# Kernel optimization log

Hardware: AMD Instinct MI355X
Metric: run time of the kernel (lower is better)

The kernel has to match this reference:

```python
import jax, jax.numpy as jnp
import numpy as np

B, S, H = 32, 512, 768          # batch, encoder seq len, hidden size
W, G = 128, 4                   # max words per example, max tokens per word group
NH, HD, FF, NL, NLAB = 4, 192, 2048, 2, 6  # heads, head dim, ffn dim, layers, labels
EPS = 1e-5


def setup_inputs() -> dict:
    key = jax.random.key(0)
    ks = jax.random.split(key, 16)
    s = 0.02
    hidden = jax.random.normal(ks[0], (B, S, H), jnp.float32)
    word_token_idx = jax.random.randint(ks[1], (B, W, G), 0, S).astype(jnp.int32)
    glen = jax.random.randint(ks[2], (B, W), 1, G + 1)
    group_token_mask = jnp.arange(G)[None, None, :] < glen[:, :, None]  # [B,W,G] bool
    nwords = jax.random.randint(ks[3], (B,), W // 2, W + 1)
    word_valid = jnp.arange(W)[None, :] < nwords[:, None]               # [B,W] bool
    return {
        'hidden': hidden,
        'word_token_idx': word_token_idx,
        'group_token_mask': group_token_mask,
        'word_valid': word_valid,
        'qkv_w': jax.random.normal(ks[4], (NL, 3 * H, H), jnp.float32) * s,
        'qkv_b': jnp.zeros((NL, 3 * H), jnp.float32),
        'out_w': jax.random.normal(ks[5], (NL, H, H), jnp.float32) * s,
        'out_b': jnp.zeros((NL, H), jnp.float32),
        'ff1_w': jax.random.normal(ks[6], (NL, FF, H), jnp.float32) * s,
        'ff1_b': jnp.zeros((NL, FF), jnp.float32),
        'ff2_w': jax.random.normal(ks[7], (NL, H, FF), jnp.float32) * s,
        'ff2_b': jnp.zeros((NL, H), jnp.float32),
        'ln1_s': jnp.ones((NL, H), jnp.float32),
        'ln1_b': jnp.zeros((NL, H), jnp.float32),
        'ln2_s': jnp.ones((NL, H), jnp.float32),
        'ln2_b': jnp.zeros((NL, H), jnp.float32),
        'cls_w': jax.random.normal(ks[8], (NLAB, H), jnp.float32) * s,
        'cls_b': jnp.zeros((NLAB,), jnp.float32),
    }


def _ln(x, s, b):
    m = x.mean(-1, keepdims=True)
    v = ((x - m) ** 2).mean(-1, keepdims=True)
    return (x - m) * jax.lax.rsqrt(v + EPS) * s + b


def reference(hidden, word_token_idx, group_token_mask, word_valid,
              qkv_w, qkv_b, out_w, out_b, ff1_w, ff1_b, ff2_w, ff2_b,
              ln1_s, ln1_b, ln2_s, ln2_b, cls_w, cls_b):
    dt = hidden.dtype
    # ragged per-word gather + masked mean over each subword group: [B,W,G,H]
    gathered = jax.vmap(lambda h, i: h[i])(hidden, word_token_idx)
    gm = group_token_mask[..., None].astype(dt)
    wemb = (gathered * gm).sum(2) / jnp.maximum(gm.sum(2), 1.0)   # [B,W,H]
    # invalid (padded) words are zero, matching torch pad_sequence zero-padding
    wemb = wemb * word_valid[..., None].astype(dt)
    cls = hidden[:, 0, :]
    x = jnp.concatenate([cls[:, None, :], wemb], axis=1)          # [B, W+1, H]
    # key padding mask: True = padded position; CLS slot always valid
    pad = jnp.concatenate([jnp.zeros((B, 1), bool), ~word_valid], axis=1)
    neg = jnp.finfo(dt).min
    Lw = W + 1
    scale = 1.0 / np.sqrt(HD)
    for l in range(NL):  # 2 post-norm TransformerEncoder layers
        qkv = x @ qkv_w[l].T + qkv_b[l]
        q, k, v = jnp.split(qkv, 3, axis=-1)
        q = q.reshape(B, Lw, NH, HD).transpose(0, 2, 1, 3)
        k = k.reshape(B, Lw, NH, HD).transpose(0, 2, 1, 3)
        v = v.reshape(B, Lw, NH, HD).transpose(0, 2, 1, 3)
        scores = jnp.einsum('bhqd,bhkd->bhqk', q, k) * scale
        scores = jnp.where(pad[:, None, None, :], neg, scores)
        a = jax.nn.softmax(scores, axis=-1)
        ctx = jnp.einsum('bhqk,bhkd->bhqd', a, v).transpose(0, 2, 1, 3).reshape(B, Lw, H)
        attn = ctx @ out_w[l].T + out_b[l]
        x = _ln(x + attn, ln1_s[l], ln1_b[l])
        h1 = jax.nn.relu(x @ ff1_w[l].T + ff1_b[l])
        x = _ln(x + h1 @ ff2_w[l].T + ff2_b[l], ln2_s[l], ln2_b[l])
    pooled = x[:, 0, :]
    logits = pooled @ cls_w.T + cls_b
    return (logits, pooled)
```

## Files before the change

### kernel.cpp

```cpp
#include <hip/hip_runtime.h>
#include <hip/hip_bf16.h>
#include <math.h>

#define B_  32
#define S_  512
#define H_  768
#define W_  128
#define G_  4
#define LW  129
#define NH_ 4
#define HD_ 192
#define FF_ 2048
#define NL_ 2
#define NLAB_ 6
#define M_   (B_ * LW)
#define MPAD 4224
#define EPS_ 1e-5f
#define SCALE_ 0.07216878364870323f

#define TP 192
#define KP 160
#define KR 144
#define KLD 200
#define PLD 168

#define QW_SZ (3 * H_ * H_)
#define OW_SZ (H_ * H_)
#define F1_SZ (FF_ * H_)
#define F2_SZ (H_ * FF_)
#define WL_SZ (QW_SZ + OW_SZ + F1_SZ + F2_SZ)

typedef __bf16 bf16_8 __attribute__((ext_vector_type(8)));
typedef float  f32x4  __attribute__((ext_vector_type(4)));
typedef unsigned short ushort8_t __attribute__((ext_vector_type(8)));

__device__ __forceinline__ float b2f(unsigned short u) {
    union { unsigned int i; float f; } c; c.i = ((unsigned int)u) << 16; return c.f;
}
__device__ __forceinline__ unsigned short f2b(float f) {
    union { float f; unsigned int u; } c; c.f = f;
    unsigned int u = c.u;
    return (unsigned short)((u + 0x7FFFu + ((u >> 16) & 1u)) >> 16);
}

__device__ __forceinline__ float wave_sum(float v) {
#pragma unroll
    for (int off = 1; off < 64; off <<= 1) v += __shfl_xor(v, off, 64);
    return v;
}
__device__ __forceinline__ float block_sum(float v, float* red) {
    v = wave_sum(v);
    int wid = threadIdx.x >> 6, lane = threadIdx.x & 63;
    if (lane == 0) red[wid] = v;
    __syncthreads();
    float r = (red[0] + red[1]) + (red[2] + red[3]);
    __syncthreads();
    return r;
}

__global__ __launch_bounds__(256) void build_x_kernel(
    const float* __restrict__ hidden,
    const int*   __restrict__ wti,
    const int*   __restrict__ gmask,
    const int*   __restrict__ wvalid,
    unsigned short* __restrict__ xb)
{
    int t = blockIdx.x;
    int b = blockIdx.y;
    int tid = threadIdx.x;
    if (t >= LW) {
        int pr = M_ + b * 3 + (t - LW);
        size_t xo = (size_t)pr * H_;
#pragma unroll
        for (int i = 0; i < 3; i++) xb[xo + tid + i * 256] = 0;
        return;
    }
    size_t xo = ((size_t)b * LW + t) * H_;
    if (t == 0) {
        const float* src = hidden + (size_t)b * S_ * H_;
#pragma unroll
        for (int i = 0; i < 3; i++) xb[xo + tid + i * 256] = f2b(src[tid + i * 256]);
    } else {
        int w = t - 1;
        int valid = wvalid[b * W_ + w];
        int ids[G_]; float msk[G_]; float cnt = 0.f;
#pragma unroll
        for (int g = 0; g < G_; g++) {
            ids[g] = wti[(b * W_ + w) * G_ + g];
            msk[g] = (gmask[(b * W_ + w) * G_ + g] != 0) ? 1.f : 0.f;
            cnt += msk[g];
        }
        float inv = valid ? (1.f / fmaxf(cnt, 1.f)) : 0.f;
#pragma unroll
        for (int i = 0; i < 3; i++) {
            int c = tid + i * 256;
            float a = 0.f;
#pragma unroll
            for (int g = 0; g < G_; g++)
                a += msk[g] * hidden[((size_t)b * S_ + ids[g]) * H_ + c];
            xb[xo + c] = f2b(a * inv);
        }
    }
}

__global__ __launch_bounds__(256) void cvt_all_kernel(
    const float4* __restrict__ qw, const float4* __restrict__ ow,
    const float4* __restrict__ f1, const float4* __restrict__ f2,
    ushort4* __restrict__ dst)
{
    constexpr int WL4 = WL_SZ / 4;
    int i = blockIdx.x * 256 + threadIdx.x;
    int l = (i < WL4) ? 0 : 1;
    int j = i - l * WL4;
    float4 v;
    if (j < QW_SZ / 4)                          v = qw[l * (QW_SZ / 4) + j];
    else if (j < (QW_SZ + OW_SZ) / 4)           v = ow[l * (OW_SZ / 4) + j - QW_SZ / 4];
    else if (j < (QW_SZ + OW_SZ + F1_SZ) / 4)   v = f1[l * (F1_SZ / 4) + j - (QW_SZ + OW_SZ) / 4];
    else                                        v = f2[l * (F2_SZ / 4) + j - (QW_SZ + OW_SZ + F1_SZ) / 4];
    ushort4 o; o.x = f2b(v.x); o.y = f2b(v.y); o.z = f2b(v.z); o.w = f2b(v.w);
    dst[i] = o;
}

template <int BM, int BN, int BK, int RELU, int OUTBF, int SWZ>
__global__ __launch_bounds__(256) void gemm_mfma(
    const unsigned short* __restrict__ A,
    const unsigned short* __restrict__ Bw,
    const float* __restrict__ bias,
    void* __restrict__ Cout,
    int N, int K)
{
    constexpr int MI  = BM / 32;
    constexpr int NJ  = BN / 32;
    constexpr int CPR = BK / 8;
    constexpr int RPL = 2048 / BK;
    constexpr int SA  = BM * BK / 2048;
    constexpr int SB  = BN * BK / 2048;

    __shared__ __align__(16) unsigned short As[BM * BK];
    __shared__ __align__(16) unsigned short Bs[BN * BK];

    const int tid  = threadIdx.x;
    const int lane = tid & 63;
    const int wid  = tid >> 6;

    int bx = blockIdx.x, by = blockIdx.y;
    if (SWZ) {
        int nx = gridDim.x;
        int total = nx * gridDim.y;
        int id = by * nx + bx;
        int id2 = (id & 7) * (total >> 3) + (id >> 3);
        by = id2 / nx; bx = id2 - by * nx;
    }
    const int bm = by * BM;
    const int bn = bx * BN;

    const int wm = (wid & 1) * (BM / 2);
    const int wn = (wid >> 1) * (BN / 2);
    const int r  = lane & 15;
    const int q8 = lane >> 4;
    const int m8 = r & (CPR - 1);

    const int srow = tid / CPR;
    const int scol = (tid % CPR) ^ (srow & (CPR - 1));
    const unsigned short* Ag = A  + (size_t)(bm + srow) * K + scol * 8;
    const unsigned short* Bg = Bw + (size_t)(bn + srow) * K + scol * 8;

    const bf16_8* Af = (const bf16_8*)As;
    const bf16_8* Bf = (const bf16_8*)Bs;
    int arow[MI], brow[NJ];
#pragma unroll
    for (int i = 0; i < MI; i++) arow[i] = (wm + i * 16 + r) * CPR;
#pragma unroll
    for (int j = 0; j < NJ; j++) brow[j] = (wn + j * 16 + r) * CPR;

    f32x4 acc[MI][NJ];
#pragma unroll
    for (int i = 0; i < MI; i++)
#pragma unroll
        for (int j = 0; j < NJ; j++) acc[i][j] = (f32x4){0.f, 0.f, 0.f, 0.f};

    for (int k0 = 0; k0 < K; k0 += BK) {
#pragma unroll
        for (int s = 0; s < SA; s++)
            __builtin_amdgcn_global_load_lds(
                (const __attribute__((address_space(1))) void*)(Ag + (size_t)(s * RPL) * K + k0),
                (__attribute__((address_space(3))) void*)(As + s * 2048 + tid * 8), 16, 0, 0);
#pragma unroll
        for (int s = 0; s < SB; s++)
            __builtin_amdgcn_global_load_lds(
                (const __attribute__((address_space(1))) void*)(Bg + (size_t)(s * RPL) * K + k0),
                (__attribute__((address_space(3))) void*)(Bs + s * 2048 + tid * 8), 16, 0, 0);
        __syncthreads();
#pragma unroll
        for (int ks = 0; ks < BK / 32; ks++) {
            const int cc = (ks * 4 + q8) ^ m8;
            bf16_8 a[MI], b[NJ];
#pragma unroll
            for (int i = 0; i < MI; i++) a[i] = Af[arow[i] + cc];
#pragma unroll
            for (int j = 0; j < NJ; j++) b[j] = Bf[brow[j] + cc];
#pragma unroll
            for (int i = 0; i < MI; i++)
#pragma unroll
                for (int j = 0; j < NJ; j++)
                    acc[i][j] = __builtin_amdgcn_mfma_f32_16x16x32_bf16(a[i], b[j], acc[i][j], 0, 0, 0);
        }
        __syncthreads();
    }

    int col[NJ]; float bv[NJ];
#pragma unroll
    for (int j = 0; j < NJ; j++) { col[j] = bn + wn + j * 16 + r; bv[j] = bias[col[j]]; }
    const int row0 = bm + wm + ((lane >> 4) << 2);
#pragma unroll
    for (int i = 0; i < MI; i++) {
#pragma unroll
        for (int rg = 0; rg < 4; rg++) {
            size_t rowoff = (size_t)(row0 + i * 16 + rg) * N;
#pragma unroll
            for (int j = 0; j < NJ; j++) {
                float v = acc[i][j][rg] + bv[j];
                if (RELU) v = fmaxf(v, 0.f);
                if (OUTBF) ((unsigned short*)Cout)[rowoff + col[j]] = f2b(v);
                else       ((float*)Cout)[rowoff + col[j]] = v;
            }
        }
    }
}

__global__ __launch_bounds__(256) void vt_kernel(
    const unsigned short* __restrict__ qkv,
    unsigned short* __restrict__ vtb)
{
    __shared__ __align__(16) unsigned short Vs[KR * KLD];
    int bh = blockIdx.x;
    int b = bh >> 2, h = bh & 3;
    int tid = threadIdx.x;
    for (int c = tid; c < KR * 24; c += 256) {
        int t = c / 24, j = c - t * 24;
        ushort8_t v = (ushort8_t){0,0,0,0,0,0,0,0};
        if (t < LW)
            v = *(const ushort8_t*)(qkv + (size_t)(b * LW + t) * (3 * H_) + 2 * H_ + h * HD_ + j * 8);
        *(ushort8_t*)(&Vs[t * KLD + j * 8]) = v;
    }
    __syncthreads();
    size_t obase = (size_t)bh * (HD_ * KP);
    for (int c = tid; c < HD_ * (KP / 4); c += 256) {
        int d = c / (KP / 4), t0 = (c - d * (KP / 4)) * 4;
        ushort4 o;
        o.x = (t0 + 0 < KR) ? Vs[(t0 + 0) * KLD + d] : 0;
        o.y = (t0 + 1 < KR) ? Vs[(t0 + 1) * KLD + d] : 0;
        o.z = (t0 + 2 < KR) ? Vs[(t0 + 2) * KLD + d] : 0;
        o.w = (t0 + 3 < KR) ? Vs[(t0 + 3) * KLD + d] : 0;
        *(ushort4*)(&vtb[obase + (size_t)d * KP + t0]) = o;
    }
}

__global__ __launch_bounds__(256) void attn_fused_kernel(
    const unsigned short* __restrict__ qkv,
    const int*            __restrict__ wvalid,
    const unsigned short* __restrict__ vtb,
    unsigned short*       __restrict__ ctx)
{
    __shared__ __align__(16) unsigned short Ks[KR * KLD];
    __shared__ __align__(16) unsigned short Ps[64 * PLD];
    __shared__ float msk[KR];
    int mb = blockIdx.x;
    int bh = blockIdx.y;
    int b = bh >> 2, h = bh & 3;
    int tid = threadIdx.x, lane = tid & 63, wid = tid >> 6;
    int q = lane >> 4, r = lane & 15;

    for (int c = tid; c < KR * 24; c += 256) {
        int t = c / 24, j = c - t * 24;
        ushort8_t v = (ushort8_t){0,0,0,0,0,0,0,0};
        if (t < LW)
            v = *(const ushort8_t*)(qkv + (size_t)(b * LW + t) * (3 * H_) + H_ + h * HD_ + j * 8);
        *(ushort8_t*)(&Ks[t * KLD + j * 8]) = v;
    }
    if (tid < KR) {
        bool valid = (tid == 0) || (tid <= W_ && wvalid[b * W_ + tid - 1] != 0);
        msk[tid] = valid ? 0.f : -1e30f;
    }
    __syncthreads();

    const int lrow0 = wid * 16;
    const unsigned short* Qp = qkv + ((size_t)(b * LW) + mb * 64 + lrow0 + r) * (3 * H_) + h * HD_;

    f32x4 acc[9];
#pragma unroll
    for (int nt = 0; nt < 9; nt++) acc[nt] = (f32x4){0.f, 0.f, 0.f, 0.f};
    for (int ks = 0; ks < HD_ / 32; ks++) {
        bf16_8 a = *(const bf16_8*)(Qp + ks * 32 + q * 8);
#pragma unroll
        for (int nt = 0; nt < 9; nt++) {
            bf16_8 bfrag = *(const bf16_8*)(&Ks[(nt * 16 + r) * KLD + ks * 32 + q * 8]);
            acc[nt] = __builtin_amdgcn_mfma_f32_16x16x32_bf16(a, bfrag, acc[nt], 0, 0, 0);
        }
    }
    float mk[9];
#pragma unroll
    for (int nt = 0; nt < 9; nt++) mk[nt] = msk[nt * 16 + r];
#pragma unroll
    for (int rg = 0; rg < 4; rg++) {
        float v[9]; float mx = -1e30f;
#pragma unroll
        for (int nt = 0; nt < 9; nt++) { v[nt] = acc[nt][rg] * SCALE_ + mk[nt]; mx = fmaxf(mx, v[nt]); }
#pragma unroll
        for (int off = 1; off < 16; off <<= 1) mx = fmaxf(mx, __shfl_xor(mx, off, 64));
        float s = 0.f;
#pragma unroll
        for (int nt = 0; nt < 9; nt++) { v[nt] = __expf(v[nt] - mx); s += v[nt]; }
#pragma unroll
        for (int off = 1; off < 16; off <<= 1) s += __shfl_xor(s, off, 64);
        float inv = 1.f / s;
        int lr = lrow0 + q * 4 + rg;
#pragma unroll
        for (int nt = 0; nt < 9; nt++)
            Ps[lr * PLD + nt * 16 + r] = f2b(v[nt] * inv);
        Ps[lr * PLD + KR + r] = 0;
    }
    __syncthreads();

    const int wm = (wid & 1) * 32, wn = (wid >> 1) * 96;
    size_t vbase = (size_t)bh * (HD_ * KP);

    f32x4 pacc[2][6];
#pragma unroll
    for (int i = 0; i < 2; i++)
#pragma unroll
        for (int j = 0; j < 6; j++) pacc[i][j] = (f32x4){0.f, 0.f, 0.f, 0.f};

    for (int ks = 0; ks < KP / 32; ks++) {
        bf16_8 a[2], bb[6];
#pragma unroll
        for (int i = 0; i < 2; i++)
            a[i] = *(const bf16_8*)(&Ps[(wm + i * 16 + r) * PLD + ks * 32 + q * 8]);
#pragma unroll
        for (int j = 0; j < 6; j++)
            bb[j] = *(const bf16_8*)(vtb + vbase + (size_t)(wn + j * 16 + r) * KP + ks * 32 + q * 8);
#pragma unroll
        for (int i = 0; i < 2; i++)
#pragma unroll
            for (int j = 0; j < 6; j++)
                pacc[i][j] = __builtin_amdgcn_mfma_f32_16x16x32_bf16(a[i], bb[j], pacc[i][j], 0, 0, 0);
    }

#pragma unroll
    for (int i = 0; i < 2; i++) {
#pragma unroll
        for (int rg = 0; rg < 4; rg++) {
            int tl = mb * 64 + wm + i * 16 + q * 4 + rg;
            if (tl < LW) {
                size_t rowoff = (size_t)(b * LW + tl) * H_ + h * HD_;
#pragma unroll
                for (int j = 0; j < 6; j++)
                    ctx[rowoff + wn + j * 16 + r] = f2b(pacc[i][j][rg]);
            }
        }
    }
}

__global__ __launch_bounds__(256) void add_ln_kernel(
    unsigned short* __restrict__ xb, const unsigned short* __restrict__ res,
    const float* __restrict__ sc, const float* __restrict__ bi)
{
    __shared__ float red[4];
    int row = blockIdx.x;
    int tid = threadIdx.x;
    size_t base = (size_t)row * H_;
    float v[3];
    float sum = 0.f;
#pragma unroll
    for (int i = 0; i < 3; i++) {
        int c = tid + i * 256;
        float t = b2f(xb[base + c]) + b2f(res[base + c]);
        v[i] = t; sum += t;
    }
    sum = block_sum(sum, red);
    float mean = sum * (1.f / H_);
    float var = 0.f;
#pragma unroll
    for (int i = 0; i < 3; i++) { float d = v[i] - mean; var += d * d; }
    var = block_sum(var, red);
    float inv = rsqrtf(var * (1.f / H_) + EPS_);
#pragma unroll
    for (int i = 0; i < 3; i++) {
        int c = tid + i * 256;
        xb[base + c] = f2b((v[i] - mean) * inv * sc[c] + bi[c]);
    }
}

__global__ __launch_bounds__(384) void cls_kernel(
    const unsigned short* __restrict__ xb,
    const float* __restrict__ cls_w, const float* __restrict__ cls_b,
    float* __restrict__ out)
{
    int b = blockIdx.x;
    int tid = threadIdx.x;
    const unsigned short* p = &xb[((size_t)b * LW) * H_];
    for (int c = tid; c < H_; c += 384) out[B_ * NLAB_ + b * H_ + c] = b2f(p[c]);
    int w = tid >> 6, lane = tid & 63;
    if (w < NLAB_) {
        const float* wv = &cls_w[w * H_];
        float acc = 0.f;
#pragma unroll
        for (int i = 0; i < H_ / 64; i++) {
            int c = lane + i * 64;
            acc += b2f(p[c]) * wv[c];
        }
        acc = wave_sum(acc);
        if (lane == 0) out[b * NLAB_ + w] = acc + cls_b[w];
    }
}

extern "C" void kernel_launch(void* const* d_in, const int* in_sizes, int n_in,
                              void* d_out, int out_size, void* d_ws, size_t ws_size,
                              hipStream_t stream) {
    const float* hidden = (const float*)d_in[0];
    const int*   wti    = (const int*)d_in[1];
    const int*   gmask  = (const int*)d_in[2];
    const int*   wvalid = (const int*)d_in[3];
    const float* qkv_w  = (const float*)d_in[4];
    const float* qkv_b  = (const float*)d_in[5];
    const float* out_w  = (const float*)d_in[6];
    const float* out_b  = (const float*)d_in[7];
    const float* ff1_w  = (const float*)d_in[8];
    const float* ff1_b  = (const float*)d_in[9];
    const float* ff2_w  = (const float*)d_in[10];
    const float* ff2_b  = (const float*)d_in[11];
    const float* ln1_s  = (const float*)d_in[12];
    const float* ln1_b  = (const float*)d_in[13];
    const float* ln2_s  = (const float*)d_in[14];
    const float* ln2_b  = (const float*)d_in[15];
    const float* cls_w  = (const float*)d_in[16];
    const float* cls_b  = (const float*)d_in[17];
    float* out = (float*)d_out;

    const size_t XSZ = (size_t)MPAD * H_;
    const size_t ASZ = (size_t)128 * TP * KP;
    unsigned short* U    = (unsigned short*)d_ws;
    unsigned short* vtb  = U;
    unsigned short* tmpb = U;
    unsigned short* xb   = U + ASZ;
    unsigned short* ctxb = xb + XSZ;
    unsigned short* qkvb = ctxb + XSZ;
    unsigned short* wb   = qkvb + (size_t)MPAD * 3 * H_;

    build_x_kernel<<<dim3(LW + 3, B_), 256, 0, stream>>>(hidden, wti, gmask, wvalid, xb);
    cvt_all_kernel<<<2 * WL_SZ / 4 / 256, 256, 0, stream>>>(
        (const float4*)qkv_w, (const float4*)out_w,
        (const float4*)ff1_w, (const float4*)ff2_w, (ushort4*)wb);

    const int GM = MPAD / 64;
    for (int l = 0; l < NL_; l++) {
        unsigned short* wbl = wb + (size_t)l * WL_SZ;
        gemm_mfma<64, 128, 64, 0, 1, 0><<<dim3(3 * H_ / 128, GM), 256, 0, stream>>>(
            xb, wbl, qkv_b + (size_t)l * 3 * H_, qkvb, 3 * H_, H_);
        vt_kernel<<<128, 256, 0, stream>>>(qkvb, vtb);
        attn_fused_kernel<<<dim3(3, 128), 256, 0, stream>>>(qkvb, wvalid, vtb, ctxb);
        gemm_mfma<64, 64, 64, 0, 1, 1><<<dim3(H_ / 64, GM), 256, 0, stream>>>(
            ctxb, wbl + QW_SZ, out_b + (size_t)l * H_, tmpb, H_, H_);
        add_ln_kernel<<<M_, 256, 0, stream>>>(xb, tmpb,
            ln1_s + (size_t)l * H_, ln1_b + (size_t)l * H_);
        gemm_mfma<64, 128, 64, 1, 1, 1><<<dim3(FF_ / 128, GM), 256, 0, stream>>>(
            xb, wbl + QW_SZ + OW_SZ, ff1_b + (size_t)l * FF_, qkvb, FF_, H_);
        gemm_mfma<64, 64, 64, 0, 1, 1><<<dim3(H_ / 64, GM), 256, 0, stream>>>(
            qkvb, wbl + QW_SZ + OW_SZ + F1_SZ, ff2_b + (size_t)l * H_, tmpb, H_, FF_);
        add_ln_kernel<<<M_, 256, 0, stream>>>(xb, tmpb,
            ln2_s + (size_t)l * H_, ln2_b + (size_t)l * H_);
    }
    cls_kernel<<<B_, 384, 0, stream>>>(xb, cls_w, cls_b, out);
    (void)in_sizes; (void)n_in; (void)out_size; (void)ws_size;
}
```

Measured before the change: 408.7 us.

## Compute only CLS row in final encoder layer with fused GEMV kernels

```diff
diff --git a/kernel.cpp b/kernel.cpp
--- a/kernel.cpp
+++ b/kernel.cpp
@@ -127,7 +127,7 @@
     const unsigned short* __restrict__ Bw,
     const float* __restrict__ bias,
     void* __restrict__ Cout,
-    int N, int K)
+    int N, int K, int ldc)
 {
     constexpr int MI  = BM / 32;
     constexpr int NJ  = BN / 32;
@@ -216,7 +216,7 @@
     for (int i = 0; i < MI; i++) {
 #pragma unroll
         for (int rg = 0; rg < 4; rg++) {
-            size_t rowoff = (size_t)(row0 + i * 16 + rg) * N;
+            size_t rowoff = (size_t)(row0 + i * 16 + rg) * ldc;
 #pragma unroll
             for (int j = 0; j < NJ; j++) {
                 float v = acc[i][j][rg] + bv[j];
@@ -391,27 +391,195 @@
     }
 }
 
-__global__ __launch_bounds__(384) void cls_kernel(
+__global__ __launch_bounds__(256) void cls_attn_kernel(
     const unsigned short* __restrict__ xb,
+    const unsigned short* __restrict__ qkvb,
+    const unsigned short* __restrict__ wq,
+    const float* __restrict__ qb,
+    const unsigned short* __restrict__ wo,
+    const float* __restrict__ ob,
+    const int* __restrict__ wvalid,
+    const float* __restrict__ ln1s, const float* __restrict__ ln1b,
+    unsigned short* __restrict__ xc)
+{
+    __shared__ float x0s[H_];
+    __shared__ float qs[H_];
+    __shared__ float ps[NH_][132];
+    __shared__ float ctxs[H_];
+    __shared__ float red[4];
+    int b = blockIdx.x;
+    int tid = threadIdx.x, lane = tid & 63, wid = tid >> 6;
+    const unsigned short* x0 = xb + (size_t)(b * LW) * H_;
+#pragma unroll
+    for (int i = 0; i < 3; i++) x0s[tid + i * 256] = b2f(x0[tid + i * 256]);
+    __syncthreads();
+#pragma unroll
+    for (int i = 0; i < 3; i++) {
+        int n = tid + i * 256;
+        const unsigned short* wr = wq + (size_t)n * H_;
+        float acc = 0.f;
+        for (int c = 0; c < H_; c += 8) {
+            ushort8_t w8 = *(const ushort8_t*)(wr + c);
+#pragma unroll
+            for (int j = 0; j < 8; j++) acc += x0s[c + j] * b2f(w8[j]);
+        }
+        qs[n] = acc + qb[n];
+    }
+    __syncthreads();
+    {
+        int h = wid;
+        const unsigned short* Kbase = qkvb + (size_t)(b * LW) * (3 * H_) + H_ + h * HD_;
+        float sc[3]; float mx = -1e30f;
+#pragma unroll
+        for (int i = 0; i < 3; i++) {
+            int t = lane + 64 * i;
+            float v = -1e30f;
+            if (t < LW) {
+                int valid = (t == 0) || (wvalid[b * W_ + t - 1] != 0);
+                const unsigned short* Kr = Kbase + (size_t)t * (3 * H_);
+                float a = 0.f;
+                for (int c = 0; c < HD_; c += 8) {
+                    ushort8_t k8 = *(const ushort8_t*)(Kr + c);
+#pragma unroll
+                    for (int j = 0; j < 8; j++) a += qs[h * HD_ + c + j] * b2f(k8[j]);
+                }
+                v = valid ? (a * SCALE_) : -1e30f;
+            }
+            sc[i] = v; mx = fmaxf(mx, v);
+        }
+#pragma unroll
+        for (int off = 1; off < 64; off <<= 1) mx = fmaxf(mx, __shfl_xor(mx, off, 64));
+        float e[3]; float s = 0.f;
+#pragma unroll
+        for (int i = 0; i < 3; i++) { e[i] = __expf(sc[i] - mx); s += e[i]; }
+#pragma unroll
+        for (int off = 1; off < 64; off <<= 1) s += __shfl_xor(s, off, 64);
+        float inv = 1.f / s;
+#pragma unroll
+        for (int i = 0; i < 3; i++) {
+            int t = lane + 64 * i;
+            if (t < LW) ps[h][t] = e[i] * inv;
+        }
+    }
+    __syncthreads();
+    {
+        int h = wid;
+        const unsigned short* Vbase = qkvb + (size_t)(b * LW) * (3 * H_) + 2 * H_ + h * HD_;
+        float cx[3] = {0.f, 0.f, 0.f};
+        for (int t = 0; t < LW; t++) {
+            float p = ps[h][t];
+            const unsigned short* Vr = Vbase + (size_t)t * (3 * H_);
+#pragma unroll
+            for (int i = 0; i < 3; i++) cx[i] += p * b2f(Vr[lane + 64 * i]);
+        }
+#pragma unroll
+        for (int i = 0; i < 3; i++) ctxs[h * HD_ + lane + 64 * i] = cx[i];
+    }
+    __syncthreads();
+    float r3[3]; float sum = 0.f;
+#pragma unroll
+    for (int i = 0; i < 3; i++) {
+        int n = tid + i * 256;
+        const unsigned short* wr = wo + (size_t)n * H_;
+        float acc = 0.f;
+        for (int c = 0; c < H_; c += 8) {
+            ushort8_t w8 = *(const ushort8_t*)(wr + c);
+#pragma unroll
+            for (int j = 0; j < 8; j++) acc += ctxs[c + j] * b2f(w8[j]);
+        }
+        float v = x0s[n] + acc + ob[n];
+        r3[i] = v; sum += v;
+    }
+    sum = block_sum(sum, red);
+    float mean = sum * (1.f / H_);
+    float var = 0.f;
+#pragma unroll
+    for (int i = 0; i < 3; i++) { float d = r3[i] - mean; var += d * d; }
+    var = block_sum(var, red);
+    float rinv = rsqrtf(var * (1.f / H_) + EPS_);
+#pragma unroll
+    for (int i = 0; i < 3; i++) {
+        int n = tid + i * 256;
+        xc[b * H_ + n] = f2b((r3[i] - mean) * rinv * ln1s[n] + ln1b[n]);
+    }
+}
+
+__global__ __launch_bounds__(256) void cls_tail_kernel(
+    const unsigned short* __restrict__ xc,
+    const unsigned short* __restrict__ f1w,
+    const float* __restrict__ f1b,
+    const unsigned short* __restrict__ f2w,
+    const float* __restrict__ f2bias,
+    const float* __restrict__ ln2s, const float* __restrict__ ln2b,
     const float* __restrict__ cls_w, const float* __restrict__ cls_b,
     float* __restrict__ out)
 {
+    __shared__ float xs[H_];
+    __shared__ unsigned short h1s[FF_];
+    __shared__ float red[4];
+    __shared__ float lred[4][NLAB_];
     int b = blockIdx.x;
-    int tid = threadIdx.x;
-    const unsigned short* p = &xb[((size_t)b * LW) * H_];
-    for (int c = tid; c < H_; c += 384) out[B_ * NLAB_ + b * H_ + c] = b2f(p[c]);
-    int w = tid >> 6, lane = tid & 63;
-    if (w < NLAB_) {
-        const float* wv = &cls_w[w * H_];
+    int tid = threadIdx.x, lane = tid & 63, wid = tid >> 6;
+#pragma unroll
+    for (int i = 0; i < 3; i++) xs[tid + i * 256] = b2f(xc[b * H_ + tid + i * 256]);
+    __syncthreads();
+#pragma unroll
+    for (int i = 0; i < 8; i++) {
+        int n = tid + i * 256;
+        const unsigned short* wr = f1w + (size_t)n * H_;
         float acc = 0.f;
-#pragma unroll
-        for (int i = 0; i < H_ / 64; i++) {
-            int c = lane + i * 64;
-            acc += b2f(p[c]) * wv[c];
-        }
-        acc = wave_sum(acc);
-        if (lane == 0) out[b * NLAB_ + w] = acc + cls_b[w];
-    }
+        for (int c = 0; c < H_; c += 8) {
+            ushort8_t w8 = *(const ushort8_t*)(wr + c);
+#pragma unroll
+            for (int j = 0; j < 8; j++) acc += xs[c + j] * b2f(w8[j]);
+        }
+        h1s[n] = f2b(fmaxf(acc + f1b[n], 0.f));
+    }
+    __syncthreads();
+    float r3[3]; float sum = 0.f;
+#pragma unroll
+    for (int i = 0; i < 3; i++) {
+        int n = tid + i * 256;
+        const unsigned short* wr = f2w + (size_t)n * FF_;
+        float acc = 0.f;
+        for (int c = 0; c < FF_; c += 8) {
+            ushort8_t w8 = *(const ushort8_t*)(wr + c);
+#pragma unroll
+            for (int j = 0; j < 8; j++) acc += b2f(h1s[c + j]) * b2f(w8[j]);
+        }
+        float v = xs[n] + acc + f2bias[n];
+        r3[i] = v; sum += v;
+    }
+    sum = block_sum(sum, red);
+    float mean = sum * (1.f / H_);
+    float var = 0.f;
+#pragma unroll
+    for (int i = 0; i < 3; i++) { float d = r3[i] - mean; var += d * d; }
+    var = block_sum(var, red);
+    float rinv = rsqrtf(var * (1.f / H_) + EPS_);
+    float f3[3];
+#pragma unroll
+    for (int i = 0; i < 3; i++) {
+        int n = tid + i * 256;
+        f3[i] = (r3[i] - mean) * rinv * ln2s[n] + ln2b[n];
+        out[B_ * NLAB_ + b * H_ + n] = f3[i];
+    }
+    float l6[NLAB_] = {0.f, 0.f, 0.f, 0.f, 0.f, 0.f};
+#pragma unroll
+    for (int i = 0; i < 3; i++) {
+        int n = tid + i * 256;
+#pragma unroll
+        for (int w = 0; w < NLAB_; w++) l6[w] += f3[i] * cls_w[w * H_ + n];
+    }
+#pragma unroll
+    for (int w = 0; w < NLAB_; w++) l6[w] = wave_sum(l6[w]);
+    if (lane == 0) {
+#pragma unroll
+        for (int w = 0; w < NLAB_; w++) lred[wid][w] = l6[w];
+    }
+    __syncthreads();
+    if (tid < NLAB_)
+        out[b * NLAB_ + tid] = lred[0][tid] + lred[1][tid] + lred[2][tid] + lred[3][tid] + cls_b[tid];
 }
 
 extern "C" void kernel_launch(void* const* d_in, const int* in_sizes, int n_in,
@@ -442,6 +610,7 @@
     unsigned short* U    = (unsigned short*)d_ws;
     unsigned short* vtb  = U;
     unsigned short* tmpb = U;
+    unsigned short* xc   = U;
     unsigned short* xb   = U + ASZ;
     unsigned short* ctxb = xb + XSZ;
     unsigned short* qkvb = ctxb + XSZ;
@@ -453,23 +622,33 @@
         (const float4*)ff1_w, (const float4*)ff2_w, (ushort4*)wb);
 
     const int GM = MPAD / 64;
-    for (int l = 0; l < NL_; l++) {
-        unsigned short* wbl = wb + (size_t)l * WL_SZ;
+
+    {
+        unsigned short* wbl = wb;
         gemm_mfma<64, 128, 64, 0, 1, 0><<<dim3(3 * H_ / 128, GM), 256, 0, stream>>>(
-            xb, wbl, qkv_b + (size_t)l * 3 * H_, qkvb, 3 * H_, H_);
+            xb, wbl, qkv_b, qkvb, 3 * H_, H_, 3 * H_);
         vt_kernel<<<128, 256, 0, stream>>>(qkvb, vtb);
         attn_fused_kernel<<<dim3(3, 128), 256, 0, stream>>>(qkvb, wvalid, vtb, ctxb);
         gemm_mfma<64, 64, 64, 0, 1, 1><<<dim3(H_ / 64, GM), 256, 0, stream>>>(
-            ctxb, wbl + QW_SZ, out_b + (size_t)l * H_, tmpb, H_, H_);
-        add_ln_kernel<<<M_, 256, 0, stream>>>(xb, tmpb,
-            ln1_s + (size_t)l * H_, ln1_b + (size_t)l * H_);
+            ctxb, wbl + QW_SZ, out_b, tmpb, H_, H_, H_);
+        add_ln_kernel<<<M_, 256, 0, stream>>>(xb, tmpb, ln1_s, ln1_b);
         gemm_mfma<64, 128, 64, 1, 1, 1><<<dim3(FF_ / 128, GM), 256, 0, stream>>>(
-            xb, wbl + QW_SZ + OW_SZ, ff1_b + (size_t)l * FF_, qkvb, FF_, H_);
+            xb, wbl + QW_SZ + OW_SZ, ff1_b, qkvb, FF_, H_, FF_);
         gemm_mfma<64, 64, 64, 0, 1, 1><<<dim3(H_ / 64, GM), 256, 0, stream>>>(
-            qkvb, wbl + QW_SZ + OW_SZ + F1_SZ, ff2_b + (size_t)l * H_, tmpb, H_, FF_);
-        add_ln_kernel<<<M_, 256, 0, stream>>>(xb, tmpb,
-            ln2_s + (size_t)l * H_, ln2_b + (size_t)l * H_);
-    }
-    cls_kernel<<<B_, 384, 0, stream>>>(xb, cls_w, cls_b, out);
+            qkvb, wbl + QW_SZ + OW_SZ + F1_SZ, ff2_b, tmpb, H_, FF_, H_);
+        add_ln_kernel<<<M_, 256, 0, stream>>>(xb, tmpb, ln2_s, ln2_b);
+    }
+
+    {
+        unsigned short* wbl = wb + WL_SZ;
+        gemm_mfma<64, 128, 64, 0, 1, 1><<<dim3(1536 / 128, GM), 256, 0, stream>>>(
+            xb, wbl + (size_t)H_ * H_, qkv_b + 3 * H_ + H_, qkvb + H_, 2 * H_, H_, 3 * H_);
+        cls_attn_kernel<<<B_, 256, 0, stream>>>(
+            xb, qkvb, wbl, qkv_b + 3 * H_, wbl + QW_SZ, out_b + H_, wvalid,
+            ln1_s + H_, ln1_b + H_, xc);
+        cls_tail_kernel<<<B_, 256, 0, stream>>>(
+            xc, wbl + QW_SZ + OW_SZ, ff1_b + FF_, wbl + QW_SZ + OW_SZ + F1_SZ, ff2_b + H_,
+            ln2_s + H_, ln2_b + H_, cls_w, cls_b, out);
+    }
     (void)in_sizes; (void)n_in; (void)out_size; (void)ws_size;
 }
```

Result: slower. 601.8 us (+47.2%).
